# Kernel tuning notes

Hardware: AMD Instinct MI355X
Metric: run time of the kernel (lower is better)

## Reference

```python
import jax, jax.numpy as jnp
import numpy as np

TEMPERATURE = 0.07
EPS = 1e-8  # torch cosine_similarity norm clamp


def setup_inputs() -> dict:
    key = jax.random.key(0)
    k1, k2 = jax.random.split(key)
    B, d = 8192, 256
    X = jax.random.normal(k1, (B, d), dtype=jnp.float32)
    Y = jax.random.normal(k2, (B, d), dtype=jnp.float32)
    return {"X": X, "Y": Y}


def _normalize(v):
    # torch cosine_similarity clamps the norm at eps
    n = jnp.sqrt(jnp.sum(v * v, axis=-1, keepdims=True))
    return v / jnp.maximum(n, EPS)


def reference(X, Y):
    # cosine similarity matrix via normalize + GEMM (same math as broadcasted
    # cosine_similarity(X.unsqueeze(1), Y.unsqueeze(0), dim=-1))
    Xn = _normalize(X)                      # [B, d]
    Yn = _normalize(Y)                      # [B, d]
    logits = (Xn @ Yn.T) / TEMPERATURE      # [B, B]
    # cross_entropy with targets = arange(B): mean of -log_softmax diagonal
    logp = jax.nn.log_softmax(logits, axis=-1)
    loss = -jnp.mean(jnp.diagonal(logp))
    return loss
```

## Files before the change

### kernel.cpp

```cpp
#include <hip/hip_runtime.h>
#include <hip/hip_bf16.h>


typedef __attribute__((ext_vector_type(2)))  float f32x2;
typedef __attribute__((ext_vector_type(4)))  float f32x4;
typedef __attribute__((ext_vector_type(4)))  int   i32x4;
typedef __attribute__((ext_vector_type(8)))  int   i32x8;

#define AS1(p) ((const __attribute__((address_space(1))) void*)(uintptr_t)(p))
#define AS3(p) ((__attribute__((address_space(3))) void*)(uintptr_t)(p))

constexpr int   BROWS = 8192;
constexpr int   DDIM  = 256;
constexpr float kInvT = 14.285714285714286f;
constexpr float kC1   = 20.609929155556622f;
constexpr float kLn2  = 0.6931471805599453f;
constexpr int   kSC   = 0x7F7F7F7F;

#if __has_builtin(__builtin_amdgcn_exp2f)
#define EXP2F(x) __builtin_amdgcn_exp2f(x)
#else
#define EXP2F(x) exp2f(x)
#endif
#if __has_builtin(__builtin_amdgcn_logf)
#define LOG2F(x) __builtin_amdgcn_logf(x)
#else
#define LOG2F(x) log2f(x)
#endif

static __device__ __forceinline__ unsigned f2fp8(float f) {
  unsigned u = __builtin_bit_cast(unsigned, f);
  unsigned s = (u >> 24) & 0x80u;
  float af = __builtin_fabsf(f);
  if (af < 0.015625f) {
    int q = (int)__builtin_rintf(af * 512.0f);
    return s | (unsigned)q;
  }
  unsigned au = u & 0x7FFFFFFFu;
  au += 0x7FFFFu + ((au >> 20) & 1u);
  unsigned e8 = ((au >> 23) - 127u + 7u) & 0xFu;
  unsigned m  = (au >> 20) & 7u;
  return s | (e8 << 3) | m;
}

__global__ __launch_bounds__(256) void nrm_kernel(
    const float* __restrict__ X, const float* __restrict__ Y,
    unsigned int* __restrict__ Xq, unsigned int* __restrict__ Yq,
    float* __restrict__ diag, float* __restrict__ row_sum)
{
  const int wave = threadIdx.x >> 6;
  const int lane = threadIdx.x & 63;
  const int row  = blockIdx.x * 4 + wave;
  const float4 x = *(const float4*)(X + (size_t)row * DDIM + lane * 4);
  const float4 y = *(const float4*)(Y + (size_t)row * DDIM + lane * 4);
  float ssx = x.x*x.x + x.y*x.y + x.z*x.z + x.w*x.w;
  float ssy = y.x*y.x + y.y*y.y + y.z*y.z + y.w*y.w;
  float dot = x.x*y.x + x.y*y.y + x.z*y.z + x.w*y.w;
  #pragma unroll
  for (int m = 1; m < 64; m <<= 1) {
    ssx += __shfl_xor(ssx, m);
    ssy += __shfl_xor(ssy, m);
    dot += __shfl_xor(dot, m);
  }
  const float invx = 1.0f / fmaxf(sqrtf(ssx), 1e-8f);
  const float invy = 1.0f / fmaxf(sqrtf(ssy), 1e-8f);
#if __has_builtin(__builtin_amdgcn_cvt_pk_fp8_f32)
  int xq = __builtin_amdgcn_cvt_pk_fp8_f32(x.x * invx, x.y * invx, 0, false);
  xq     = __builtin_amdgcn_cvt_pk_fp8_f32(x.z * invx, x.w * invx, xq, true);
  int yq = __builtin_amdgcn_cvt_pk_fp8_f32(y.x * invy, y.y * invy, 0, false);
  yq     = __builtin_amdgcn_cvt_pk_fp8_f32(y.z * invy, y.w * invy, yq, true);
#else
  int xq = (int)(f2fp8(x.x*invx) | (f2fp8(x.y*invx) << 8) |
                 (f2fp8(x.z*invx) << 16) | (f2fp8(x.w*invx) << 24));
  int yq = (int)(f2fp8(y.x*invy) | (f2fp8(y.y*invy) << 8) |
                 (f2fp8(y.z*invy) << 16) | (f2fp8(y.w*invy) << 24));
#endif
  Xq[row * 64 + lane] = (unsigned)xq;
  Yq[row * 64 + lane] = (unsigned)yq;
  if (lane == 0) {
    diag[row] = dot * invx * invy * kInvT;
    row_sum[row] = 0.0f;
  }
}

static __device__ __forceinline__ void expflush(f32x4 (&pm)[2], f32x2 (&sm)[2]) {
  #pragma unroll
  for (int n = 0; n < 2; ++n) {
    f32x2 v0 = { pm[n][0], pm[n][1] };
    f32x2 v1 = { pm[n][2], pm[n][3] };
    v0 = v0 * kC1 + (f32x2){-kC1, -kC1};
    v1 = v1 * kC1 + (f32x2){-kC1, -kC1};
    sm[0] += (f32x2){ EXP2F(v0.x), EXP2F(v0.y) };
    sm[1] += (f32x2){ EXP2F(v1.x), EXP2F(v1.y) };
  }
}

static __device__ __forceinline__ void tile_step(
    const char* __restrict__ tb, const int (&bb)[2][2], const i32x8 (&a)[4][2],
    f32x4 (&cur)[4][2], f32x4 (&prev)[4][2], f32x2 (&sums2)[4][2])
{
  i32x8 b[2];
  __builtin_amdgcn_s_setprio(1);
  #pragma unroll
  for (int n = 0; n < 2; ++n) {
    const i32x4 lo = *(const i32x4*)(tb + bb[n][0]);
    const i32x4 hi = *(const i32x4*)(tb + bb[n][1]);
    b[n] = __builtin_shufflevector(lo, hi, 0, 1, 2, 3, 4, 5, 6, 7);
  }
  #pragma unroll
  for (int m = 0; m < 4; ++m) {
    cur[m][0] = __builtin_amdgcn_mfma_scale_f32_16x16x128_f8f6f4(
        a[m][0], b[0], (f32x4){0.f, 0.f, 0.f, 0.f}, 0, 0, 0, kSC, 0, kSC);
    cur[m][1] = __builtin_amdgcn_mfma_scale_f32_16x16x128_f8f6f4(
        a[m][0], b[1], (f32x4){0.f, 0.f, 0.f, 0.f}, 0, 0, 0, kSC, 0, kSC);
  }
  __builtin_amdgcn_s_setprio(0);
  expflush(prev[0], sums2[0]);
  expflush(prev[1], sums2[1]);
  __builtin_amdgcn_s_setprio(1);
  #pragma unroll
  for (int n = 0; n < 2; ++n) {
    const i32x4 lo = *(const i32x4*)(tb + bb[n][0] + 128);
    const i32x4 hi = *(const i32x4*)(tb + bb[n][1] + 128);
    b[n] = __builtin_shufflevector(lo, hi, 0, 1, 2, 3, 4, 5, 6, 7);
  }
  #pragma unroll
  for (int m = 0; m < 4; ++m) {
    cur[m][0] = __builtin_amdgcn_mfma_scale_f32_16x16x128_f8f6f4(
        a[m][1], b[0], cur[m][0], 0, 0, 0, kSC, 0, kSC);
    cur[m][1] = __builtin_amdgcn_mfma_scale_f32_16x16x128_f8f6f4(
        a[m][1], b[1], cur[m][1], 0, 0, 0, kSC, 0, kSC);
  }
  __builtin_amdgcn_s_setprio(0);
  expflush(prev[2], sums2[2]);
  expflush(prev[3], sums2[3]);
}

__global__ __launch_bounds__(256, 2) void logits_kernel(
    const unsigned char* __restrict__ Xq,
    const unsigned char* __restrict__ Yq,
    float* __restrict__ row_sum)
{
  __shared__ char lds[4 * 8192];
  const int tid  = threadIdx.x;
  const int lane = tid & 63;
  const int wave = tid >> 6;
  const int l15  = lane & 15;
  const int g    = lane >> 4;

  const int bid  = blockIdx.x;
  const int xcd  = bid & 7;
  const int idx  = bid >> 3;
  const int panel = (xcd >> 2) * 16 + (idx & 15);
  const int split = (xcd & 3) * 4 + (idx >> 4);

  const int rowbase = panel * 256 + wave * 64;
  const char* Xb = (const char*)Xq;
  const char* Yb = (const char*)Yq + (size_t)split * (512 * 256);

  i32x8 a[4][2];
  #pragma unroll
  for (int m = 0; m < 4; ++m) {
    const char* rp = Xb + (size_t)(rowbase + m * 16 + l15) * 256 + g * 32;
    a[m][0] = *(const i32x8*)(rp);
    a[m][1] = *(const i32x8*)(rp + 128);
  }

  f32x2 sums2[4][2];
  #pragma unroll
  for (int m = 0; m < 4; ++m) {
    sums2[m][0] = (f32x2){0.f, 0.f};
    sums2[m][1] = (f32x2){0.f, 0.f};
  }

  const int sr = (l15 & 7) << 4;
  const int gx = (g * 32) ^ sr;
  int bb[2][2];
  #pragma unroll
  for (int n = 0; n < 2; ++n) {
    bb[n][0] = (n * 16 + l15) * 256 + gx;
    bb[n][1] = bb[n][0] ^ 16;
  }

  auto stage = [&](int t, int b) {
    const char* Yt = Yb + (size_t)t * 8192;
    char* db = lds + b * 8192;
    #pragma unroll
    for (int s = 0; s < 2; ++s) {
      const int portion = wave * 2048 + s * 1024;
      const int L = portion + lane * 16;
      const int src = (L & ~255) | ((L & 255) ^ (((L >> 8) & 7) << 4));
      __builtin_amdgcn_global_load_lds(AS1(Yt + src), AS3(db + portion), 16, 0, 0);
    }
  };

  f32x4 accA[4][2], accB[4][2];
  #pragma unroll
  for (int m = 0; m < 4; ++m)
    #pragma unroll
    for (int n = 0; n < 2; ++n) {
      accA[m][n] = (f32x4){0.f, 0.f, 0.f, 0.f};
      const float ni = -__builtin_inff();
      accB[m][n] = (f32x4){ni, ni, ni, ni};
    }

  stage(0, 0);
  stage(1, 1);
  #pragma unroll 1
  for (int q = 0; q < 4; ++q) {
    const int j = 4 * q;
    asm volatile("s_waitcnt vmcnt(0)" ::: "memory");
    __builtin_amdgcn_s_barrier();
    stage(j + 2, 2);
    tile_step(lds + 0 * 8192, bb, a, accA, accB, sums2);
    stage(j + 3, 3);
    tile_step(lds + 1 * 8192, bb, a, accB, accA, sums2);
    asm volatile("s_waitcnt vmcnt(0)" ::: "memory");
    __builtin_amdgcn_s_barrier();
    if (q < 3) stage(j + 4, 0);
    tile_step(lds + 2 * 8192, bb, a, accA, accB, sums2);
    if (q < 3) stage(j + 5, 1);
    tile_step(lds + 3 * 8192, bb, a, accB, accA, sums2);
  }
  #pragma unroll
  for (int m = 0; m < 4; ++m)
    expflush(accB[m], sums2[m]);

  #pragma unroll
  for (int m = 0; m < 4; ++m)
    #pragma unroll
    for (int h = 0; h < 2; ++h)
      #pragma unroll
      for (int r2 = 0; r2 < 2; ++r2) {
        float s = (r2 == 0) ? sums2[m][h].x : sums2[m][h].y;
        s += __shfl_xor(s, 1);
        s += __shfl_xor(s, 2);
        s += __shfl_xor(s, 4);
        s += __shfl_xor(s, 8);
        if (l15 == 0)
          atomicAdd(row_sum + rowbase + m * 16 + g * 4 + h * 2 + r2, s);
      }
}

__global__ __launch_bounds__(1024) void loss_kernel(
    const float* __restrict__ row_sum, const float* __restrict__ diag,
    float* __restrict__ out)
{
  const int t = threadIdx.x;
  double acc = 0.0;
  #pragma unroll
  for (int h = 0; h < 2; ++h) {
    const int i = h * 4096 + t * 4;
    const float4 s = *(const float4*)(row_sum + i);
    const float4 d = *(const float4*)(diag + i);
    acc += (double)(kInvT + LOG2F(s.x) * kLn2 - d.x);
    acc += (double)(kInvT + LOG2F(s.y) * kLn2 - d.y);
    acc += (double)(kInvT + LOG2F(s.z) * kLn2 - d.z);
    acc += (double)(kInvT + LOG2F(s.w) * kLn2 - d.w);
  }
  #pragma unroll
  for (int m = 1; m < 64; m <<= 1) acc += __shfl_xor(acc, m);
  __shared__ double red[16];
  if ((t & 63) == 0) red[t >> 6] = acc;
  __syncthreads();
  if (t == 0) {
    double tot = 0.0;
    #pragma unroll
    for (int w = 0; w < 16; ++w) tot += red[w];
    out[0] = (float)(tot / (double)BROWS);
  }
}

extern "C" void kernel_launch(void* const* d_in, const int* in_sizes, int n_in,
                              void* d_out, int out_size, void* d_ws, size_t ws_size,
                              hipStream_t stream) {
  (void)in_sizes; (void)n_in; (void)out_size; (void)ws_size;
  const float* X = (const float*)d_in[0];
  const float* Y = (const float*)d_in[1];
  char* w = (char*)d_ws;
  unsigned int* Xq = (unsigned int*)(w);
  unsigned int* Yq = (unsigned int*)(w + (2u << 20));
  float* diag    = (float*)(w + (4u << 20));
  float* row_sum = (float*)(w + (4u << 20) + (32u << 10));

  nrm_kernel<<<BROWS / 4, 256, 0, stream>>>(X, Y, Xq, Yq, diag, row_sum);
  logits_kernel<<<512, 256, 0, stream>>>((const unsigned char*)Xq,
                                         (const unsigned char*)Yq, row_sum);
  loss_kernel<<<1, 1024, 0, stream>>>(row_sum, diag, (float*)d_out);
}
```

Before: 35.32 us.

## Give each wave private double-buffered LDS staging and drop block barriers

Each wave now loads the full Y tile into its own private pair of 8 KB LDS buffers instead of sharing four block-wide buffers filled cooperatively. Tile readiness is tracked with per-wave vmcnt waits, so the s_barrier calls between stages are removed. This targets cross-wave synchronisation stalls, but each wave now issues four times the global loads and LDS use doubles to 64 KB per block, which may reduce occupancy below the two blocks per CU in the launch bounds and increases L2 traffic.

```diff
diff --git a/kernel.cpp b/kernel.cpp
--- a/kernel.cpp
+++ b/kernel.cpp
@@ -141,7 +141,7 @@
     const unsigned char* __restrict__ Yq,
     float* __restrict__ row_sum)
 {
-  __shared__ char lds[4 * 8192];
+  __shared__ char lds[4 * 16384];
   const int tid  = threadIdx.x;
   const int lane = tid & 63;
   const int wave = tid >> 6;
@@ -157,6 +157,7 @@
   const int rowbase = panel * 256 + wave * 64;
   const char* Xb = (const char*)Xq;
   const char* Yb = (const char*)Yq + (size_t)split * (512 * 256);
+  char* myb = lds + wave * 16384;
 
   i32x8 a[4][2];
   #pragma unroll
@@ -182,15 +183,14 @@
     bb[n][1] = bb[n][0] ^ 16;
   }
 
-  auto stage = [&](int t, int b) {
+  auto stage = [&](int t, int buf) {
     const char* Yt = Yb + (size_t)t * 8192;
-    char* db = lds + b * 8192;
-    #pragma unroll
-    for (int s = 0; s < 2; ++s) {
-      const int portion = wave * 2048 + s * 1024;
-      const int L = portion + lane * 16;
+    char* db = myb + buf * 8192;
+    #pragma unroll
+    for (int s = 0; s < 8; ++s) {
+      const int L = s * 1024 + lane * 16;
       const int src = (L & ~255) | ((L & 255) ^ (((L >> 8) & 7) << 4));
-      __builtin_amdgcn_global_load_lds(AS1(Yt + src), AS3(db + portion), 16, 0, 0);
+      __builtin_amdgcn_global_load_lds(AS1(Yt + src), AS3(db + s * 1024), 16, 0, 0);
     }
   };
 
@@ -207,20 +207,20 @@
   stage(0, 0);
   stage(1, 1);
   #pragma unroll 1
-  for (int q = 0; q < 4; ++q) {
-    const int j = 4 * q;
-    asm volatile("s_waitcnt vmcnt(0)" ::: "memory");
-    __builtin_amdgcn_s_barrier();
-    stage(j + 2, 2);
-    tile_step(lds + 0 * 8192, bb, a, accA, accB, sums2);
-    stage(j + 3, 3);
-    tile_step(lds + 1 * 8192, bb, a, accB, accA, sums2);
-    asm volatile("s_waitcnt vmcnt(0)" ::: "memory");
-    __builtin_amdgcn_s_barrier();
-    if (q < 3) stage(j + 4, 0);
-    tile_step(lds + 2 * 8192, bb, a, accA, accB, sums2);
-    if (q < 3) stage(j + 5, 1);
-    tile_step(lds + 3 * 8192, bb, a, accB, accA, sums2);
+  for (int p = 0; p < 8; ++p) {
+    const int t = 2 * p;
+    asm volatile("s_waitcnt vmcnt(8)" ::: "memory");
+    tile_step(myb, bb, a, accA, accB, sums2);
+    __builtin_amdgcn_sched_barrier(0);
+    if (t + 2 < 16) stage(t + 2, 0);
+    if (p < 7) {
+      asm volatile("s_waitcnt vmcnt(8)" ::: "memory");
+    } else {
+      asm volatile("s_waitcnt vmcnt(0)" ::: "memory");
+    }
+    tile_step(myb + 8192, bb, a, accB, accA, sums2);
+    __builtin_amdgcn_sched_barrier(0);
+    if (t + 3 < 16) stage(t + 3, 1);
   }
   #pragma unroll
   for (int m = 0; m < 4; ++m)
```

Measured after the change: 36.59 us. 3.6% more time.

## Deepen LDS prefetch pipeline to three tiles ahead with partial vmcnt waits

Applied to the files above, without the earlier changes.

The tile loop becomes a rolling 4-buffer ring with three tiles prefetched ahead. It waits with vmcnt(4) instead of draining all outstanding loads before each barrier, so global->LDS copies overlap more of the MFMA work. The LDS swizzle is also changed to XOR over 16 row groups with a rearranged per-wave portion layout, and B addresses are derived by XOR from one base offset. This aims to cut load stalls and LDS bank conflicts, but it relies on the vmcnt counting matching the number of issued loads exactly.

```diff
diff --git a/kernel.cpp b/kernel.cpp
--- a/kernel.cpp
+++ b/kernel.cpp
@@ -96,15 +96,15 @@
 }
 
 static __device__ __forceinline__ void tile_step(
-    const char* __restrict__ tb, const int (&bb)[2][2], const i32x8 (&a)[4][2],
+    const char* __restrict__ tb, const int (&bb)[2], const i32x8 (&a)[4][2],
     f32x4 (&cur)[4][2], f32x4 (&prev)[4][2], f32x2 (&sums2)[4][2])
 {
   i32x8 b[2];
   __builtin_amdgcn_s_setprio(1);
   #pragma unroll
   for (int n = 0; n < 2; ++n) {
-    const i32x4 lo = *(const i32x4*)(tb + bb[n][0]);
-    const i32x4 hi = *(const i32x4*)(tb + bb[n][1]);
+    const i32x4 lo = *(const i32x4*)(tb + (bb[n]));
+    const i32x4 hi = *(const i32x4*)(tb + (bb[n] ^ 16));
     b[n] = __builtin_shufflevector(lo, hi, 0, 1, 2, 3, 4, 5, 6, 7);
   }
   #pragma unroll
@@ -120,8 +120,8 @@
   __builtin_amdgcn_s_setprio(1);
   #pragma unroll
   for (int n = 0; n < 2; ++n) {
-    const i32x4 lo = *(const i32x4*)(tb + bb[n][0] + 128);
-    const i32x4 hi = *(const i32x4*)(tb + bb[n][1] + 128);
+    const i32x4 lo = *(const i32x4*)(tb + (bb[n] ^ 128));
+    const i32x4 hi = *(const i32x4*)(tb + (bb[n] ^ 144));
     b[n] = __builtin_shufflevector(lo, hi, 0, 1, 2, 3, 4, 5, 6, 7);
   }
   #pragma unroll
@@ -173,23 +173,19 @@
     sums2[m][1] = (f32x2){0.f, 0.f};
   }
 
-  const int sr = (l15 & 7) << 4;
-  const int gx = (g * 32) ^ sr;
-  int bb[2][2];
-  #pragma unroll
-  for (int n = 0; n < 2; ++n) {
-    bb[n][0] = (n * 16 + l15) * 256 + gx;
-    bb[n][1] = bb[n][0] ^ 16;
-  }
-
-  auto stage = [&](int t, int b) {
+  int bb[2];
+  #pragma unroll
+  for (int n = 0; n < 2; ++n)
+    bb[n] = (n * 16 + l15) * 256 + (((2 * g) ^ l15) << 4);
+
+  auto stage = [&](int t, int buf) {
     const char* Yt = Yb + (size_t)t * 8192;
-    char* db = lds + b * 8192;
+    char* db = lds + buf * 8192;
     #pragma unroll
     for (int s = 0; s < 2; ++s) {
-      const int portion = wave * 2048 + s * 1024;
+      const int portion = (s * 4 + wave) * 1024;
       const int L = portion + lane * 16;
-      const int src = (L & ~255) | ((L & 255) ^ (((L >> 8) & 7) << 4));
+      const int src = (L & ~255) | ((L & 255) ^ (((L >> 8) & 15) << 4));
       __builtin_amdgcn_global_load_lds(AS1(Yt + src), AS3(db + portion), 16, 0, 0);
     }
   };
@@ -206,21 +202,20 @@
 
   stage(0, 0);
   stage(1, 1);
+  stage(2, 2);
   #pragma unroll 1
-  for (int q = 0; q < 4; ++q) {
-    const int j = 4 * q;
-    asm volatile("s_waitcnt vmcnt(0)" ::: "memory");
+  for (int p = 0; p < 8; ++p) {
+    const int t = 2 * p;
+    if (p < 7) asm volatile("s_waitcnt vmcnt(4)" ::: "memory");
+    else       asm volatile("s_waitcnt vmcnt(2)" ::: "memory");
     __builtin_amdgcn_s_barrier();
-    stage(j + 2, 2);
-    tile_step(lds + 0 * 8192, bb, a, accA, accB, sums2);
-    stage(j + 3, 3);
-    tile_step(lds + 1 * 8192, bb, a, accB, accA, sums2);
-    asm volatile("s_waitcnt vmcnt(0)" ::: "memory");
+    if (t + 3 < 16) stage(t + 3, (t + 3) & 3);
+    tile_step(lds + (t & 3) * 8192, bb, a, accA, accB, sums2);
+    if (p < 7) asm volatile("s_waitcnt vmcnt(4)" ::: "memory");
+    else       asm volatile("s_waitcnt vmcnt(0)" ::: "memory");
     __builtin_amdgcn_s_barrier();
-    if (q < 3) stage(j + 4, 0);
-    tile_step(lds + 2 * 8192, bb, a, accA, accB, sums2);
-    if (q < 3) stage(j + 5, 1);
-    tile_step(lds + 3 * 8192, bb, a, accB, accA, sums2);
+    if (t + 4 < 16) stage(t + 4, (t + 4) & 3);
+    tile_step(lds + ((t + 1) & 3) * 8192, bb, a, accB, accA, sums2);
   }
   #pragma unroll
   for (int m = 0; m < 4; ++m)
```

Measured after the change: 34.77 us, median of 2. No clear change (-1.6%).
